# Optimization experiments

Measured on AMD Instinct MI355X. Metric: run time of the kernel, lower is better.

Reference implementation:

```python
import jax, jax.numpy as jnp
import numpy as np

B, S, D, H = 2, 2048, 768, 12
HD = D // H
WINDOW = 64  # local_attention // 2
ROPE_THETA = 10000.0
NEG = -1e9


def setup_inputs() -> dict:
    key = jax.random.key(0)
    k1, k2, k3 = jax.random.split(key, 3)
    hidden_states = jax.random.normal(k1, (B, S, D), dtype=jnp.float32)
    Wqkv_w = jax.random.normal(k2, (3 * D, D), dtype=jnp.float32) * (D ** -0.5)
    Wo_w = jax.random.normal(k3, (D, D), dtype=jnp.float32) * (D ** -0.5)
    position_ids = jnp.broadcast_to(jnp.arange(S, dtype=jnp.int64 if jax.config.jax_enable_x64 else jnp.int32), (B, S))
    # additive sliding-window mask: 0 inside window, -1e9 outside (matches torch ModernBert mask construction)
    idx = np.arange(S)
    dist = np.abs(idx[:, None] - idx[None, :])
    sliding_window_mask = jnp.asarray(np.where(dist <= WINDOW, 0.0, NEG), dtype=jnp.float32)[None, None]  # [1,1,S,S]
    return {"hidden_states": hidden_states, "Wqkv_w": Wqkv_w, "Wo_w": Wo_w,
            "sliding_window_mask": sliding_window_mask, "position_ids": position_ids}


def _rotate_half(x):
    x1, x2 = jnp.split(x, 2, axis=-1)
    return jnp.concatenate([-x2, x1], axis=-1)


def reference(hidden_states, Wqkv_w, Wo_w, sliding_window_mask, position_ids):
    b, s, d = hidden_states.shape
    qkv = hidden_states @ Wqkv_w.T                      # [B,S,3D]
    qkv = qkv.reshape(b, s, 3, H, HD)
    q = qkv[:, :, 0].transpose(0, 2, 1, 3)              # [B,H,S,HD]
    k = qkv[:, :, 1].transpose(0, 2, 1, 3)
    v = qkv[:, :, 2].transpose(0, 2, 1, 3)
    # RoPE
    inv_freq = 1.0 / (ROPE_THETA ** (jnp.arange(0, HD, 2, dtype=jnp.float32) / HD))  # [HD/2]
    freqs = position_ids.astype(jnp.float32)[..., None] * inv_freq                   # [B,S,HD/2]
    emb = jnp.concatenate([freqs, freqs], axis=-1)                                   # [B,S,HD]
    cos = jnp.cos(emb)[:, None]                          # [B,1,S,HD]
    sin = jnp.sin(emb)[:, None]
    q = q * cos + _rotate_half(q) * sin
    k = k * cos + _rotate_half(k) * sin
    scale = HD ** -0.5
    scores = jnp.einsum('bhqd,bhkd->bhqk', q, k) * scale + sliding_window_mask       # [B,H,S,S]
    attn = jax.nn.softmax(scores.astype(jnp.float32), axis=-1).astype(q.dtype)
    out = jnp.einsum('bhqk,bhkd->bhqd', attn, v)         # [B,H,S,HD]
    out = out.transpose(0, 2, 1, 3).reshape(b, s, d)     # [B,S,D]
    return out @ Wo_w.T
```

## Files before the change

### kernel.cpp

```cpp
#include <hip/hip_runtime.h>
#include <hip/hip_bf16.h>
#include <cmath>

#define B_   2
#define S_   2048
#define D_   768
#define H_   12
#define HD_  64
#define WIN_ 64

typedef __bf16 bf16x8 __attribute__((ext_vector_type(8)));
typedef __bf16 bf16x4 __attribute__((ext_vector_type(4)));
typedef float  f32x4  __attribute__((ext_vector_type(4)));
typedef unsigned int u32;

__device__ __forceinline__ void async_ld16(const void* g, void* l) {
    __builtin_amdgcn_global_load_lds(
        (__attribute__((address_space(1))) void*)(size_t)g,
        (__attribute__((address_space(3))) void*)(u32)(size_t)l,
        16, 0, 0);
}

#define WAIT_VM0   0x0F70
#define WAIT_LGKM0 0xC07F

#define NHS (B_ * S_ * D_)
#define NWQ (3 * D_ * D_)
#define NWO (D_ * D_)

__global__ __launch_bounds__(256) void to_bf16_3(const float* __restrict__ a,
                                                 const float* __restrict__ b,
                                                 const float* __restrict__ c,
                                                 __bf16* __restrict__ oa,
                                                 __bf16* __restrict__ ob,
                                                 __bf16* __restrict__ oc) {
    const int NA = NHS / 4, NB = NWQ / 4;
    int v = blockIdx.x * 256 + threadIdx.x;
    const float* src; __bf16* dst; int idx;
    if (v < NA)           { src = a; dst = oa; idx = v; }
    else if (v < NA + NB) { src = b; dst = ob; idx = v - NA; }
    else                  { src = c; dst = oc; idx = v - NA - NB; }
    float4 x = ((const float4*)src)[idx];
    bf16x4 y = { (__bf16)x.x, (__bf16)x.y, (__bf16)x.z, (__bf16)x.w };
    *(bf16x4*)(dst + (size_t)idx * 4) = y;
}

template <int MODE, int SPLIT>
__global__ __launch_bounds__(64 * SPLIT) void gemm_s(const __bf16* __restrict__ A,
                                                     const __bf16* __restrict__ Bw,
                                                     float* __restrict__ C,
                                                     __bf16* __restrict__ qkv,
                                                     __bf16* __restrict__ vt,
                                                     const int* __restrict__ pos,
                                                     int M, int N, int K) {
    __shared__ __attribute__((aligned(16))) char smem[SPLIT * 8192];

    const int tid  = threadIdx.x;
    const int w    = tid >> 6;
    const int lane = tid & 63;
    const int m0 = blockIdx.y * 64;
    const int n0 = blockIdx.x * 64;
    const int fr = lane & 15, fq = lane >> 4;
    const int sw = (fq + (fr >> 1)) & 3;

    __bf16* As = (__bf16*)(smem + w * 8192);
    __bf16* Bs = As + 2048;

    f32x4 acc[4][4] = {};

    const int nkw = (K / SPLIT) >> 5;
    const int kbase = w * (K / SPLIT);

    for (int ki = 0; ki < nkw; ++ki) {
        const int k0 = kbase + (ki << 5);
        __builtin_amdgcn_s_waitcnt(WAIT_LGKM0);
        #pragma unroll
        for (int i = 0; i < 4; ++i) {
            const int c = i * 64 + lane;
            const int row = c >> 2, ccp = c & 3;
            const int cc = (ccp - (row >> 1)) & 3;
            async_ld16(A  + (size_t)(m0 + row) * K + k0 + cc * 8, As + c * 8);
            async_ld16(Bw + (size_t)(n0 + row) * K + k0 + cc * 8, Bs + c * 8);
        }
        __builtin_amdgcn_s_waitcnt(WAIT_VM0);

        bf16x8 af[4], bfv[4];
        #pragma unroll
        for (int t = 0; t < 4; ++t) {
            af[t]  = *(const bf16x8*)(As + (t * 16 + fr) * 32 + sw * 8);
            bfv[t] = *(const bf16x8*)(Bs + (t * 16 + fr) * 32 + sw * 8);
        }
        #pragma unroll
        for (int ti = 0; ti < 4; ++ti)
            #pragma unroll
            for (int tj = 0; tj < 4; ++tj)
                acc[ti][tj] = __builtin_amdgcn_mfma_f32_16x16x32_bf16(
                    af[ti], bfv[tj], acc[ti][tj], 0, 0, 0);
    }

    float* red0 = (float*)smem;
    float* red1 = (float*)smem + 4096;

    __syncthreads();
    if (SPLIT == 2) {
        if (w == 1) {
            #pragma unroll
            for (int ti = 0; ti < 4; ++ti)
                #pragma unroll
                for (int tj = 0; tj < 4; ++tj)
                    *(f32x4*)(red0 + (ti * 4 + tj) * 256 + lane * 4) = acc[ti][tj];
        }
        __syncthreads();
        if (w == 0) {
            #pragma unroll
            for (int ti = 0; ti < 4; ++ti)
                #pragma unroll
                for (int tj = 0; tj < 4; ++tj)
                    acc[ti][tj] += *(const f32x4*)(red0 + (ti * 4 + tj) * 256 + lane * 4);
        }
    } else {
        if (w == 1 || w == 3) {
            float* rb = (w == 1) ? red0 : red1;
            #pragma unroll
            for (int ti = 0; ti < 4; ++ti)
                #pragma unroll
                for (int tj = 0; tj < 4; ++tj)
                    *(f32x4*)(rb + (ti * 4 + tj) * 256 + lane * 4) = acc[ti][tj];
        }
        __syncthreads();
        if (w == 0 || w == 2) {
            float* rb = (w == 0) ? red0 : red1;
            #pragma unroll
            for (int ti = 0; ti < 4; ++ti)
                #pragma unroll
                for (int tj = 0; tj < 4; ++tj)
                    acc[ti][tj] += *(const f32x4*)(rb + (ti * 4 + tj) * 256 + lane * 4);
        }
        __syncthreads();
        if (w == 2) {
            #pragma unroll
            for (int ti = 0; ti < 4; ++ti)
                #pragma unroll
                for (int tj = 0; tj < 4; ++tj)
                    *(f32x4*)(red0 + (ti * 4 + tj) * 256 + lane * 4) = acc[ti][tj];
        }
        __syncthreads();
        if (w == 0) {
            #pragma unroll
            for (int ti = 0; ti < 4; ++ti)
                #pragma unroll
                for (int tj = 0; tj < 4; ++tj)
                    acc[ti][tj] += *(const f32x4*)(red0 + (ti * 4 + tj) * 256 + lane * 4);
        }
    }

    if (w != 0) return;

    if (MODE == 0) {
        #pragma unroll
        for (int ti = 0; ti < 4; ++ti)
            #pragma unroll
            for (int tj = 0; tj < 4; ++tj) {
                const int col = n0 + tj * 16 + fr;
                #pragma unroll
                for (int r = 0; r < 4; ++r) {
                    const int row = m0 + ti * 16 + fq * 4 + r;
                    C[(size_t)row * N + col] = acc[ti][tj][r];
                }
            }
    } else {
        if (n0 < 2 * D_) {
            const float invf0 = __powf(10000.0f, -(float)fr * (1.0f / 32.0f));
            const float invf1 = __powf(10000.0f, -(float)(16 + fr) * (1.0f / 32.0f));
            #pragma unroll
            for (int ti = 0; ti < 4; ++ti)
                #pragma unroll
                for (int r = 0; r < 4; ++r) {
                    const int row = m0 + ti * 16 + fq * 4 + r;
                    const float p = (float)pos[row];
                    float s0, c0, s1, c1;
                    __sincosf(p * invf0, &s0, &c0);
                    __sincosf(p * invf1, &s1, &c1);
                    const float x0 = acc[ti][0][r], x1 = acc[ti][2][r];
                    acc[ti][0][r] = x0 * c0 - x1 * s0;
                    acc[ti][2][r] = x1 * c0 + x0 * s0;
                    const float y0 = acc[ti][1][r], y1 = acc[ti][3][r];
                    acc[ti][1][r] = y0 * c1 - y1 * s1;
                    acc[ti][3][r] = y1 * c1 + y0 * s1;
                }
            #pragma unroll
            for (int ti = 0; ti < 4; ++ti)
                #pragma unroll
                for (int tj = 0; tj < 4; ++tj) {
                    const int col = n0 + tj * 16 + fr;
                    #pragma unroll
                    for (int r = 0; r < 4; ++r) {
                        const int row = m0 + ti * 16 + fq * 4 + r;
                        qkv[(size_t)row * (2 * D_) + col] = (__bf16)acc[ti][tj][r];
                    }
                }
        } else {
            const int h = (n0 - 2 * D_) >> 6;
            #pragma unroll
            for (int ti = 0; ti < 4; ++ti)
                #pragma unroll
                for (int tj = 0; tj < 4; ++tj) {
                    const int d = tj * 16 + fr;
                    const int row0 = m0 + ti * 16 + fq * 4;
                    const int bb = row0 >> 11, t0 = row0 & (S_ - 1);
                    bf16x4 pk = { (__bf16)acc[ti][tj][0], (__bf16)acc[ti][tj][1],
                                  (__bf16)acc[ti][tj][2], (__bf16)acc[ti][tj][3] };
                    *(bf16x4*)(vt + ((size_t)((bb * H_ + h) * HD_ + d)) * S_ + t0) = pk;
                }
        }
    }
}

__global__ __launch_bounds__(256) void attn_mfma(const __bf16* __restrict__ qkv,
                                                 const __bf16* __restrict__ vt,
                                                 __bf16* __restrict__ outb) {
    __shared__ __attribute__((aligned(16))) __bf16 smem[24576];
    __bf16* Ks  = smem;
    __bf16* Vts = smem + 12288;

    const int i0  = blockIdx.x * 64;
    const int h   = blockIdx.y;
    const int b   = blockIdx.z;
    const int tid = threadIdx.x;
    const int w = tid >> 6, lane = tid & 63;
    const int fr = lane & 15, fq = lane >> 4;
    const int wq0 = w * 16;

    #pragma unroll
    for (int i = 0; i < 6; ++i) {
        int c = i * 256 + tid;
        int ks = (i >= 3);
        int rem = c - ks * 768;
        int cc = rem & 3, row = rem >> 2;
        int j = i0 - 64 + row; j = min(max(j, 0), S_ - 1);
        async_ld16(qkv + ((size_t)b * S_ + j) * (2 * D_) + D_ + h * HD_ + ks * 32 + cc * 8,
                   Ks + c * 8);
    }
    const size_t vbase = (size_t)((b * H_ + h) * HD_) * S_;
    #pragma unroll
    for (int i = 0; i < 6; ++i) {
        int c = i * 256 + tid;
        int ks = c >> 8, rem = c & 255, d = rem >> 2, cc = rem & 3;
        int key = i0 - 64 + ks * 32 + cc * 8;
        key = min(max(key, 0), S_ - 8);
        async_ld16(vt + vbase + (size_t)d * S_ + key, Vts + c * 8);
    }

    const size_t qrow = ((size_t)b * S_ + i0 + wq0 + fr) * (2 * D_) + h * HD_;
    bf16x8 aq[2];
    aq[0] = *(const bf16x8*)(qkv + qrow + fq * 8);
    aq[1] = *(const bf16x8*)(qkv + qrow + 32 + fq * 8);

    __syncthreads();

    f32x4 sc[12] = {};
    #pragma unroll
    for (int nt = 0; nt < 12; ++nt) {
        #pragma unroll
        for (int ks = 0; ks < 2; ++ks) {
            bf16x8 bk = *(const bf16x8*)(Ks + (ks * 192 + nt * 16 + fr) * 32 + fq * 8);
            sc[nt] = __builtin_amdgcn_mfma_f32_16x16x32_bf16(aq[ks], bk, sc[nt], 0, 0, 0);
        }
    }

    float mx[4] = { -1e30f, -1e30f, -1e30f, -1e30f };
    #pragma unroll
    for (int nt = 0; nt < 12; ++nt) {
        const int jr = nt * 16 + fr;
        const int j  = i0 - 64 + jr;
        const bool jv = (j >= 0) && (j < S_);
        #pragma unroll
        for (int r = 0; r < 4; ++r) {
            const int ir = wq0 + fq * 4 + r + 64;
            const int dd = ir - jr;
            const bool v = jv && (dd <= WIN_) && (dd >= -WIN_);
            sc[nt][r] = v ? sc[nt][r] * 0.125f : -1e30f;
            mx[r] = fmaxf(mx[r], sc[nt][r]);
        }
    }
    #pragma unroll
    for (int r = 0; r < 4; ++r)
        #pragma unroll
        for (int off = 1; off < 16; off <<= 1)
            mx[r] = fmaxf(mx[r], __shfl_xor(mx[r], off, 64));

    float sm[4] = { 0.f, 0.f, 0.f, 0.f };
    #pragma unroll
    for (int nt = 0; nt < 12; ++nt)
        #pragma unroll
        for (int r = 0; r < 4; ++r) {
            float e = __expf(sc[nt][r] - mx[r]);
            sc[nt][r] = e;
            sm[r] += e;
        }
    #pragma unroll
    for (int r = 0; r < 4; ++r) {
        #pragma unroll
        for (int off = 1; off < 16; off <<= 1)
            sm[r] += __shfl_xor(sm[r], off, 64);
        sm[r] = 1.0f / sm[r];
    }

    __syncthreads();

    __bf16* Pw = Ks + w * 3072;
    #pragma unroll
    for (int nt = 0; nt < 12; ++nt) {
        const int ks = nt >> 1, kk = (nt & 1) * 16 + fr;
        #pragma unroll
        for (int r = 0; r < 4; ++r)
            Pw[(ks * 16 + fq * 4 + r) * 32 + kk] = (__bf16)(sc[nt][r] * sm[r]);
    }

    f32x4 oacc[4] = {};
    #pragma unroll
    for (int ks = 0; ks < 6; ++ks) {
        bf16x8 ap = *(const bf16x8*)(Pw + (ks * 16 + fr) * 32 + fq * 8);
        #pragma unroll
        for (int nt2 = 0; nt2 < 4; ++nt2) {
            bf16x8 bv = *(const bf16x8*)(Vts + (ks * 64 + nt2 * 16 + fr) * 32 + fq * 8);
            oacc[nt2] = __builtin_amdgcn_mfma_f32_16x16x32_bf16(ap, bv, oacc[nt2], 0, 0, 0);
        }
    }

    const size_t obase = ((size_t)b * S_ + i0 + wq0) * D_ + h * HD_;
    #pragma unroll
    for (int nt2 = 0; nt2 < 4; ++nt2)
        #pragma unroll
        for (int r = 0; r < 4; ++r)
            outb[obase + (size_t)(fq * 4 + r) * D_ + nt2 * 16 + fr] = (__bf16)oacc[nt2][r];
}

extern "C" void kernel_launch(void* const* d_in, const int* in_sizes, int n_in,
                              void* d_out, int out_size, void* d_ws, size_t ws_size,
                              hipStream_t stream) {
    const float* hs   = (const float*)d_in[0];
    const float* wqkv = (const float*)d_in[1];
    const float* wo   = (const float*)d_in[2];
    const int*   pos  = (const int*)d_in[4];
    float* out = (float*)d_out;

    __bf16* base    = (__bf16*)d_ws;
    __bf16* hs_bf   = base;
    __bf16* wqkv_bf = hs_bf + NHS;
    __bf16* wo_bf   = wqkv_bf + NWQ;
    __bf16* qkv     = wo_bf + NWO;
    __bf16* vt      = qkv + (size_t)(B_ * S_) * (2 * D_);
    __bf16* attn_bf = vt + (size_t)B_ * H_ * HD_ * S_;

    to_bf16_3<<<(NHS + NWQ + NWO) / 1024, 256, 0, stream>>>(
        hs, wqkv, wo, hs_bf, wqkv_bf, wo_bf);

    gemm_s<1, 2><<<dim3((3 * D_) / 64, (B_ * S_) / 64), 128, 0, stream>>>(
        hs_bf, wqkv_bf, nullptr, qkv, vt, pos, B_ * S_, 3 * D_, D_);

    attn_mfma<<<dim3(S_ / 64, H_, B_), 256, 0, stream>>>(qkv, vt, attn_bf);

    gemm_s<0, 4><<<dim3(D_ / 64, (B_ * S_) / 64), 256, 0, stream>>>(
        attn_bf, wo_bf, out, nullptr, nullptr, nullptr, B_ * S_, D_, D_);
}
```

Measured before the change: 154.5 us.

## Fuse fp32-to-bf16 conversion into GEMM loads and coalesce epilogue stores via LDS

Drops the separate conversion kernel: both GEMMs now stream fp32 inputs straight into LDS through async loads and pack them to bf16 when building MFMA fragments. Epilogues for the output, QKV, V-transpose and attention output are staged through padded LDS so global stores become wide, coalesced vector writes instead of scattered scalar ones. The split-K reduction is simplified into a serial loop. In exchange each GEMM moves twice the bytes per fp32 tile, uses more LDS, and re-converts the weights in every block.

```diff
diff --git a/kernel.cpp b/kernel.cpp
--- a/kernel.cpp
+++ b/kernel.cpp
@@ -24,71 +24,94 @@
 #define WAIT_VM0   0x0F70
 #define WAIT_LGKM0 0xC07F
 
-#define NHS (B_ * S_ * D_)
-#define NWQ (3 * D_ * D_)
-#define NWO (D_ * D_)
-
-__global__ __launch_bounds__(256) void to_bf16_3(const float* __restrict__ a,
-                                                 const float* __restrict__ b,
-                                                 const float* __restrict__ c,
-                                                 __bf16* __restrict__ oa,
-                                                 __bf16* __restrict__ ob,
-                                                 __bf16* __restrict__ oc) {
-    const int NA = NHS / 4, NB = NWQ / 4;
-    int v = blockIdx.x * 256 + threadIdx.x;
-    const float* src; __bf16* dst; int idx;
-    if (v < NA)           { src = a; dst = oa; idx = v; }
-    else if (v < NA + NB) { src = b; dst = ob; idx = v - NA; }
-    else                  { src = c; dst = oc; idx = v - NA - NB; }
-    float4 x = ((const float4*)src)[idx];
-    bf16x4 y = { (__bf16)x.x, (__bf16)x.y, (__bf16)x.z, (__bf16)x.w };
-    *(bf16x4*)(dst + (size_t)idx * 4) = y;
-}
-
-template <int MODE, int SPLIT>
-__global__ __launch_bounds__(64 * SPLIT) void gemm_s(const __bf16* __restrict__ A,
-                                                     const __bf16* __restrict__ Bw,
-                                                     float* __restrict__ C,
-                                                     __bf16* __restrict__ qkv,
-                                                     __bf16* __restrict__ vt,
-                                                     const int* __restrict__ pos,
-                                                     int M, int N, int K) {
-    __shared__ __attribute__((aligned(16))) char smem[SPLIT * 8192];
-
-    const int tid  = threadIdx.x;
-    const int w    = tid >> 6;
-    const int lane = tid & 63;
+__device__ __forceinline__ bf16x8 pack8(f32x4 a, f32x4 b) {
+    bf16x8 r = { (__bf16)a[0], (__bf16)a[1], (__bf16)a[2], (__bf16)a[3],
+                 (__bf16)b[0], (__bf16)b[1], (__bf16)b[2], (__bf16)b[3] };
+    return r;
+}
+
+template <int MODE, int SPLIT, int AF32, int BF32>
+__global__ __launch_bounds__(64 * SPLIT) void gemm_f(
+        const void* __restrict__ Av, const void* __restrict__ Bv,
+        float* __restrict__ C, __bf16* __restrict__ qkv, __bf16* __restrict__ vt,
+        const int* __restrict__ pos, int M, int N, int K) {
+    constexpr int ABYTES = AF32 ? 8192 : 4096;
+    constexpr int BBYTES = BF32 ? 8192 : 4096;
+    constexpr int WBYTES = ABYTES + BBYTES;
+    __shared__ __attribute__((aligned(16))) char smem[SPLIT * WBYTES];
+
+    const int tid = threadIdx.x;
+    const int w = tid >> 6, lane = tid & 63;
     const int m0 = blockIdx.y * 64;
     const int n0 = blockIdx.x * 64;
     const int fr = lane & 15, fq = lane >> 4;
-    const int sw = (fq + (fr >> 1)) & 3;
-
-    __bf16* As = (__bf16*)(smem + w * 8192);
-    __bf16* Bs = As + 2048;
+
+    char* As = smem + w * WBYTES;
+    char* Bs = As + ABYTES;
 
     f32x4 acc[4][4] = {};
-
     const int nkw = (K / SPLIT) >> 5;
     const int kbase = w * (K / SPLIT);
 
     for (int ki = 0; ki < nkw; ++ki) {
         const int k0 = kbase + (ki << 5);
         __builtin_amdgcn_s_waitcnt(WAIT_LGKM0);
-        #pragma unroll
-        for (int i = 0; i < 4; ++i) {
-            const int c = i * 64 + lane;
-            const int row = c >> 2, ccp = c & 3;
-            const int cc = (ccp - (row >> 1)) & 3;
-            async_ld16(A  + (size_t)(m0 + row) * K + k0 + cc * 8, As + c * 8);
-            async_ld16(Bw + (size_t)(n0 + row) * K + k0 + cc * 8, Bs + c * 8);
+        if (AF32) {
+            const float* Af = (const float*)Av;
+            #pragma unroll
+            for (int i = 0; i < 8; ++i) {
+                int c = i * 64 + lane, row = c >> 3, ch = c & 7;
+                int cc = (ch - row) & 7;
+                async_ld16(Af + (size_t)(m0 + row) * K + k0 + cc * 4, As + c * 16);
+            }
+        } else {
+            const __bf16* Ab = (const __bf16*)Av;
+            #pragma unroll
+            for (int i = 0; i < 4; ++i) {
+                int c = i * 64 + lane, row = c >> 2, ch = c & 3;
+                int cc = (ch - row) & 3;
+                async_ld16(Ab + (size_t)(m0 + row) * K + k0 + cc * 8, As + c * 16);
+            }
+        }
+        if (BF32) {
+            const float* Bf = (const float*)Bv;
+            #pragma unroll
+            for (int i = 0; i < 8; ++i) {
+                int c = i * 64 + lane, row = c >> 3, ch = c & 7;
+                int cc = (ch - row) & 7;
+                async_ld16(Bf + (size_t)(n0 + row) * K + k0 + cc * 4, Bs + c * 16);
+            }
+        } else {
+            const __bf16* Bb = (const __bf16*)Bv;
+            #pragma unroll
+            for (int i = 0; i < 4; ++i) {
+                int c = i * 64 + lane, row = c >> 2, ch = c & 3;
+                int cc = (ch - row) & 3;
+                async_ld16(Bb + (size_t)(n0 + row) * K + k0 + cc * 8, Bs + c * 16);
+            }
         }
         __builtin_amdgcn_s_waitcnt(WAIT_VM0);
 
         bf16x8 af[4], bfv[4];
         #pragma unroll
         for (int t = 0; t < 4; ++t) {
-            af[t]  = *(const bf16x8*)(As + (t * 16 + fr) * 32 + sw * 8);
-            bfv[t] = *(const bf16x8*)(Bs + (t * 16 + fr) * 32 + sw * 8);
+            const int row = t * 16 + fr;
+            if (AF32) {
+                const float* rA = (const float*)As + row * 32;
+                const int p0 = (2 * fq + row) & 7, p1 = (p0 + 1) & 7;
+                af[t] = pack8(*(const f32x4*)(rA + p0 * 4), *(const f32x4*)(rA + p1 * 4));
+            } else {
+                const __bf16* rA = (const __bf16*)As + row * 32;
+                af[t] = *(const bf16x8*)(rA + ((fq + row) & 3) * 8);
+            }
+            if (BF32) {
+                const float* rB = (const float*)Bs + row * 32;
+                const int p0 = (2 * fq + row) & 7, p1 = (p0 + 1) & 7;
+                bfv[t] = pack8(*(const f32x4*)(rB + p0 * 4), *(const f32x4*)(rB + p1 * 4));
+            } else {
+                const __bf16* rB = (const __bf16*)Bs + row * 32;
+                bfv[t] = *(const bf16x8*)(rB + ((fq + row) & 3) * 8);
+            }
         }
         #pragma unroll
         for (int ti = 0; ti < 4; ++ti)
@@ -98,17 +121,16 @@
                     af[ti], bfv[tj], acc[ti][tj], 0, 0, 0);
     }
 
-    float* red0 = (float*)smem;
-    float* red1 = (float*)smem + 4096;
-
+    float* red = (float*)(smem + SPLIT * WBYTES - 16384);
     __syncthreads();
-    if (SPLIT == 2) {
-        if (w == 1) {
+    #pragma unroll
+    for (int src = 1; src < SPLIT; ++src) {
+        if (w == src) {
             #pragma unroll
             for (int ti = 0; ti < 4; ++ti)
                 #pragma unroll
                 for (int tj = 0; tj < 4; ++tj)
-                    *(f32x4*)(red0 + (ti * 4 + tj) * 256 + lane * 4) = acc[ti][tj];
+                    *(f32x4*)(red + (ti * 4 + tj) * 256 + lane * 4) = acc[ti][tj];
         }
         __syncthreads();
         if (w == 0) {
@@ -116,102 +138,77 @@
             for (int ti = 0; ti < 4; ++ti)
                 #pragma unroll
                 for (int tj = 0; tj < 4; ++tj)
-                    acc[ti][tj] += *(const f32x4*)(red0 + (ti * 4 + tj) * 256 + lane * 4);
+                    acc[ti][tj] += *(const f32x4*)(red + (ti * 4 + tj) * 256 + lane * 4);
+        }
+        __syncthreads();
+    }
+    if (w != 0) return;
+
+    if (MODE == 0) {
+        float* eL = (float*)smem;
+        #pragma unroll
+        for (int ti = 0; ti < 4; ++ti)
+            #pragma unroll
+            for (int tj = 0; tj < 4; ++tj)
+                #pragma unroll
+                for (int r = 0; r < 4; ++r)
+                    eL[(ti * 16 + fq * 4 + r) * 65 + tj * 16 + fr] = acc[ti][tj][r];
+        #pragma unroll
+        for (int p = 0; p < 16; ++p) {
+            const int rc = p * 4 + (lane >> 4), ch = lane & 15;
+            f32x4 vv = *(const f32x4*)(eL + rc * 65 + ch * 4);
+            *(f32x4*)(C + (size_t)(m0 + rc) * N + n0 + ch * 4) = vv;
+        }
+    } else if (n0 < 2 * D_) {
+        const float invf0 = __powf(10000.0f, -(float)fr * (1.0f / 32.0f));
+        const float invf1 = __powf(10000.0f, -(float)(16 + fr) * (1.0f / 32.0f));
+        #pragma unroll
+        for (int ti = 0; ti < 4; ++ti)
+            #pragma unroll
+            for (int r = 0; r < 4; ++r) {
+                const int row = m0 + ti * 16 + fq * 4 + r;
+                const float p = (float)pos[row];
+                float s0, c0, s1, c1;
+                __sincosf(p * invf0, &s0, &c0);
+                __sincosf(p * invf1, &s1, &c1);
+                const float x0 = acc[ti][0][r], x1 = acc[ti][2][r];
+                acc[ti][0][r] = x0 * c0 - x1 * s0;
+                acc[ti][2][r] = x1 * c0 + x0 * s0;
+                const float y0 = acc[ti][1][r], y1 = acc[ti][3][r];
+                acc[ti][1][r] = y0 * c1 - y1 * s1;
+                acc[ti][3][r] = y1 * c1 + y0 * s1;
+            }
+        __bf16* eL = (__bf16*)smem;
+        #pragma unroll
+        for (int ti = 0; ti < 4; ++ti)
+            #pragma unroll
+            for (int tj = 0; tj < 4; ++tj)
+                #pragma unroll
+                for (int r = 0; r < 4; ++r)
+                    eL[(ti * 16 + fq * 4 + r) * 68 + tj * 16 + fr] = (__bf16)acc[ti][tj][r];
+        #pragma unroll
+        for (int p = 0; p < 8; ++p) {
+            const int rq = p * 8 + (lane >> 3), ch = lane & 7;
+            bf16x8 vv = *(const bf16x8*)(eL + rq * 68 + ch * 8);
+            *(bf16x8*)(qkv + (size_t)(m0 + rq) * (2 * D_) + n0 + ch * 8) = vv;
         }
     } else {
-        if (w == 1 || w == 3) {
-            float* rb = (w == 1) ? red0 : red1;
-            #pragma unroll
-            for (int ti = 0; ti < 4; ++ti)
-                #pragma unroll
-                for (int tj = 0; tj < 4; ++tj)
-                    *(f32x4*)(rb + (ti * 4 + tj) * 256 + lane * 4) = acc[ti][tj];
-        }
-        __syncthreads();
-        if (w == 0 || w == 2) {
-            float* rb = (w == 0) ? red0 : red1;
-            #pragma unroll
-            for (int ti = 0; ti < 4; ++ti)
-                #pragma unroll
-                for (int tj = 0; tj < 4; ++tj)
-                    acc[ti][tj] += *(const f32x4*)(rb + (ti * 4 + tj) * 256 + lane * 4);
-        }
-        __syncthreads();
-        if (w == 2) {
-            #pragma unroll
-            for (int ti = 0; ti < 4; ++ti)
-                #pragma unroll
-                for (int tj = 0; tj < 4; ++tj)
-                    *(f32x4*)(red0 + (ti * 4 + tj) * 256 + lane * 4) = acc[ti][tj];
-        }
-        __syncthreads();
-        if (w == 0) {
-            #pragma unroll
-            for (int ti = 0; ti < 4; ++ti)
-                #pragma unroll
-                for (int tj = 0; tj < 4; ++tj)
-                    acc[ti][tj] += *(const f32x4*)(red0 + (ti * 4 + tj) * 256 + lane * 4);
-        }
-    }
-
-    if (w != 0) return;
-
-    if (MODE == 0) {
-        #pragma unroll
-        for (int ti = 0; ti < 4; ++ti)
-            #pragma unroll
-            for (int tj = 0; tj < 4; ++tj) {
-                const int col = n0 + tj * 16 + fr;
-                #pragma unroll
-                for (int r = 0; r < 4; ++r) {
-                    const int row = m0 + ti * 16 + fq * 4 + r;
-                    C[(size_t)row * N + col] = acc[ti][tj][r];
-                }
-            }
-    } else {
-        if (n0 < 2 * D_) {
-            const float invf0 = __powf(10000.0f, -(float)fr * (1.0f / 32.0f));
-            const float invf1 = __powf(10000.0f, -(float)(16 + fr) * (1.0f / 32.0f));
-            #pragma unroll
-            for (int ti = 0; ti < 4; ++ti)
-                #pragma unroll
-                for (int r = 0; r < 4; ++r) {
-                    const int row = m0 + ti * 16 + fq * 4 + r;
-                    const float p = (float)pos[row];
-                    float s0, c0, s1, c1;
-                    __sincosf(p * invf0, &s0, &c0);
-                    __sincosf(p * invf1, &s1, &c1);
-                    const float x0 = acc[ti][0][r], x1 = acc[ti][2][r];
-                    acc[ti][0][r] = x0 * c0 - x1 * s0;
-                    acc[ti][2][r] = x1 * c0 + x0 * s0;
-                    const float y0 = acc[ti][1][r], y1 = acc[ti][3][r];
-                    acc[ti][1][r] = y0 * c1 - y1 * s1;
-                    acc[ti][3][r] = y1 * c1 + y0 * s1;
-                }
-            #pragma unroll
-            for (int ti = 0; ti < 4; ++ti)
-                #pragma unroll
-                for (int tj = 0; tj < 4; ++tj) {
-                    const int col = n0 + tj * 16 + fr;
-                    #pragma unroll
-                    for (int r = 0; r < 4; ++r) {
-                        const int row = m0 + ti * 16 + fq * 4 + r;
-                        qkv[(size_t)row * (2 * D_) + col] = (__bf16)acc[ti][tj][r];
-                    }
-                }
-        } else {
-            const int h = (n0 - 2 * D_) >> 6;
-            #pragma unroll
-            for (int ti = 0; ti < 4; ++ti)
-                #pragma unroll
-                for (int tj = 0; tj < 4; ++tj) {
-                    const int d = tj * 16 + fr;
-                    const int row0 = m0 + ti * 16 + fq * 4;
-                    const int bb = row0 >> 11, t0 = row0 & (S_ - 1);
-                    bf16x4 pk = { (__bf16)acc[ti][tj][0], (__bf16)acc[ti][tj][1],
-                                  (__bf16)acc[ti][tj][2], (__bf16)acc[ti][tj][3] };
-                    *(bf16x4*)(vt + ((size_t)((bb * H_ + h) * HD_ + d)) * S_ + t0) = pk;
-                }
+        const int h = (n0 - 2 * D_) >> 6;
+        const int bb = m0 >> 11, t0 = m0 & (S_ - 1);
+        __bf16* eL = (__bf16*)smem;
+        #pragma unroll
+        for (int ti = 0; ti < 4; ++ti)
+            #pragma unroll
+            for (int tj = 0; tj < 4; ++tj)
+                #pragma unroll
+                for (int r = 0; r < 4; ++r)
+                    eL[(tj * 16 + fr) * 68 + ti * 16 + fq * 4 + r] = (__bf16)acc[ti][tj][r];
+        const size_t vb = (size_t)((bb * H_ + h) * HD_) * S_ + t0;
+        #pragma unroll
+        for (int p = 0; p < 8; ++p) {
+            const int d = p * 8 + (lane >> 3), ch = lane & 7;
+            bf16x8 vv = *(const bf16x8*)(eL + d * 68 + ch * 8);
+            *(bf16x8*)(vt + vb + (size_t)d * S_ + ch * 8) = vv;
         }
     }
 }
@@ -328,12 +325,17 @@
         }
     }
 
-    const size_t obase = ((size_t)b * S_ + i0 + wq0) * D_ + h * HD_;
     #pragma unroll
     for (int nt2 = 0; nt2 < 4; ++nt2)
         #pragma unroll
         for (int r = 0; r < 4; ++r)
-            outb[obase + (size_t)(fq * 4 + r) * D_ + nt2 * 16 + fr] = (__bf16)oacc[nt2][r];
+            Pw[(fq * 4 + r) * 68 + nt2 * 16 + fr] = (__bf16)oacc[nt2][r];
+    #pragma unroll
+    for (int p = 0; p < 2; ++p) {
+        const int q = p * 8 + (lane >> 3), ch = lane & 7;
+        bf16x8 vv = *(const bf16x8*)(Pw + q * 68 + ch * 8);
+        *(bf16x8*)(outb + ((size_t)b * S_ + i0 + wq0 + q) * D_ + h * HD_ + ch * 8) = vv;
+    }
 }
 
 extern "C" void kernel_launch(void* const* d_in, const int* in_sizes, int n_in,
@@ -345,22 +347,15 @@
     const int*   pos  = (const int*)d_in[4];
     float* out = (float*)d_out;
 
-    __bf16* base    = (__bf16*)d_ws;
-    __bf16* hs_bf   = base;
-    __bf16* wqkv_bf = hs_bf + NHS;
-    __bf16* wo_bf   = wqkv_bf + NWQ;
-    __bf16* qkv     = wo_bf + NWO;
+    __bf16* qkv     = (__bf16*)d_ws;
     __bf16* vt      = qkv + (size_t)(B_ * S_) * (2 * D_);
     __bf16* attn_bf = vt + (size_t)B_ * H_ * HD_ * S_;
 
-    to_bf16_3<<<(NHS + NWQ + NWO) / 1024, 256, 0, stream>>>(
-        hs, wqkv, wo, hs_bf, wqkv_bf, wo_bf);
-
-    gemm_s<1, 2><<<dim3((3 * D_) / 64, (B_ * S_) / 64), 128, 0, stream>>>(
-        hs_bf, wqkv_bf, nullptr, qkv, vt, pos, B_ * S_, 3 * D_, D_);
+    gemm_f<1, 2, 1, 1><<<dim3((3 * D_) / 64, (B_ * S_) / 64), 128, 0, stream>>>(
+        hs, wqkv, nullptr, qkv, vt, pos, B_ * S_, 3 * D_, D_);
 
     attn_mfma<<<dim3(S_ / 64, H_, B_), 256, 0, stream>>>(qkv, vt, attn_bf);
 
-    gemm_s<0, 4><<<dim3(D_ / 64, (B_ * S_) / 64), 256, 0, stream>>>(
-        attn_bf, wo_bf, out, nullptr, nullptr, nullptr, B_ * S_, D_, D_);
-}
+    gemm_f<0, 4, 0, 1><<<dim3(D_ / 64, (B_ * S_) / 64), 256, 0, stream>>>(
+        attn_bf, wo, out, nullptr, nullptr, nullptr, B_ * S_, D_, D_);
+}
```

Measured after the change: 170.5 us. +10.4%, slower.
